# Optimization experiments

Hardware: AMD Instinct MI355X
Metric: run time of the kernel (lower is better)

Reference implementation:

```python
import jax, jax.numpy as jnp
import numpy as np
from jax import lax

TAU = 2.0          # spikingjelly LIFNode default tau
VTH = 1.0          # v_threshold
ALPHA = 2.0        # ATan surrogate alpha (grad only; fwd is heaviside)
N_WIN = (2, 4, 4)
TOPK = 4
HEADS = 8
EPS = 1e-5


@jax.custom_vjp
def spike(x):
    return (x >= 0).astype(x.dtype)

def _spike_fwd(x):
    return (x >= 0).astype(x.dtype), x

def _spike_bwd(x, g):
    sg = (ALPHA / 2.0) / (1.0 + (jnp.pi / 2.0 * ALPHA * x) ** 2)
    return (g * sg,)

spike.defvjp(_spike_fwd, _spike_bwd)


def lif(x_seq):
    # multi-step LIF, v_reset=None (soft reset), decay_input=True, detach_reset
    def step(v, x):
        v = v + (x - v) / TAU
        s = spike(v - VTH)
        v = v - lax.stop_gradient(s) * VTH
        return v, s
    v0 = jnp.zeros_like(x_seq[0])
    _, s_seq = lax.scan(step, v0, x_seq)
    return s_seq


def bn3d(x, g, b):
    # track_running_stats=False -> always batch stats; step_mode 'm' folds T into batch.
    # x: [T,B,C,Lt,Lh,Lw]; normalize per-channel over (T,B,Lt,Lh,Lw)
    ax = (0, 1, 3, 4, 5)
    m = x.mean(ax, keepdims=True)
    v = x.var(ax, keepdims=True)
    sh = (1, 1, -1, 1, 1, 1)
    return g.reshape(sh) * (x - m) * lax.rsqrt(v + EPS) + b.reshape(sh)


def bra(x, wqkv, bqkv, lepe_w, wo, bo):
    # Bi-level routing attention over 3D windows. x: [N, Lt, Lh, Lw, C]
    N, Lt, Lh, Lw, C = x.shape
    nt, nh, nw = N_WIN
    rt, rh, rw = Lt // nt, Lh // nh, Lw // nw
    R, P = nt * nh * nw, rt * rh * rw
    Dh = C // HEADS

    qkv = x @ wqkv + bqkv                       # [N,Lt,Lh,Lw,3C]
    q, k, v = jnp.split(qkv, 3, axis=-1)

    def to_reg(t):  # -> [N, R, P, C]
        t = t.reshape(N, nt, rt, nh, rh, nw, rw, C)
        return t.transpose(0, 1, 3, 5, 2, 4, 6, 7).reshape(N, R, P, C)

    def from_reg(t):  # [N,R,P,C] -> [N,Lt,Lh,Lw,C]
        t = t.reshape(N, nt, nh, nw, rt, rh, rw, C)
        return t.transpose(0, 1, 4, 2, 5, 3, 6, 7).reshape(N, Lt, Lh, Lw, C)

    qr, kr, vr = to_reg(q), to_reg(k), to_reg(v)

    # coarse routing: region means, top-k region selection
    a_r = jnp.einsum('nrc,nsc->nrs', qr.mean(2), kr.mean(2))   # [N,R,R]
    _, idx = lax.top_k(a_r, TOPK)                               # [N,R,TOPK]

    # gather selected regions' k,v: [N,R,TOPK,P,C] -> [N,R,TOPK*P,H,Dh]
    kg = jax.vmap(lambda a, i: a[i])(kr, idx)
    vg = jax.vmap(lambda a, i: a[i])(vr, idx)
    kg = kg.reshape(N, R, TOPK * P, HEADS, Dh)
    vg = vg.reshape(N, R, TOPK * P, HEADS, Dh)
    qh = qr.reshape(N, R, P, HEADS, Dh)

    logits = jnp.einsum('nrphd,nrkhd->nrhpk', qh * (Dh ** -0.5), kg)
    attn = jax.nn.softmax(logits, axis=-1)
    out = jnp.einsum('nrhpk,nrkhd->nrphd', attn, vg).reshape(N, R, P, C)
    out = from_reg(out)

    # LEPE: depthwise 3x3x3 conv on v
    v_ncdhw = v.transpose(0, 4, 1, 2, 3)
    lepe = lax.conv_general_dilated(
        v_ncdhw, lepe_w, (1, 1, 1), 'SAME', feature_group_count=C,
        dimension_numbers=('NCDHW', 'OIDHW', 'NCDHW'))
    out = out + lepe.transpose(0, 2, 3, 4, 1)

    return out @ wo + bo


def setup_inputs() -> dict:
    key = jax.random.key(0)
    ks = jax.random.split(key, 8)
    T, B, C, Lt, Lh, Lw = 2, 1, 256, 8, 32, 32
    inp = {
        'x': jax.random.normal(ks[0], (T, B, C, Lt, Lh, Lw), jnp.float32),
        'bn1_g': jnp.ones((C,), jnp.float32),
        'bn1_b': jnp.zeros((C,), jnp.float32),
        'wqkv': jax.random.normal(ks[1], (C, 3 * C), jnp.float32) * (C ** -0.5),
        'bqkv': jnp.zeros((3 * C,), jnp.float32),
        'lepe_w': jax.random.normal(ks[2], (C, 1, 3, 3, 3), jnp.float32) * 0.1,
        'wo': jax.random.normal(ks[3], (C, C), jnp.float32) * (C ** -0.5),
        'bo': jnp.zeros((C,), jnp.float32),
        'bn2_g': jnp.ones((C,), jnp.float32),
        'bn2_b': jnp.zeros((C,), jnp.float32),
        'ffn_w1': jax.random.normal(ks[4], (C, 4 * C), jnp.float32) * (C ** -0.5),
        'ffn_b1': jnp.zeros((4 * C,), jnp.float32),
        'ffn_w2': jax.random.normal(ks[5], (4 * C, C), jnp.float32) * ((4 * C) ** -0.5),
        'ffn_b2': jnp.zeros((C,), jnp.float32),
        'scale': jnp.ones((1,), jnp.float32) * 0.5,
    }
    return inp


def reference(x, bn1_g, bn1_b, wqkv, bqkv, lepe_w, wo, bo,
              bn2_g, bn2_b, ffn_w1, ffn_b1, ffn_w2, ffn_b2, scale):
    T, B, C, Lt, Lh, Lw = x.shape

    # --- attention branch ---
    s1 = lif(bn3d(x, bn1_g, bn1_b))                       # [T,B,C,Lt,Lh,Lw]
    sa = s1.transpose(0, 1, 3, 4, 5, 2).reshape(T * B, Lt, Lh, Lw, C)
    a = bra(sa, wqkv, bqkv, lepe_w, wo, bo)
    a = a.reshape(T, B, Lt, Lh, Lw, C).transpose(0, 1, 5, 2, 3, 4)
    x = x + a * scale

    # --- FFN branch (1x1x1 conv = channel GEMM) ---
    s2 = lif(bn3d(x, bn2_g, bn2_b))
    h = jax.nn.gelu(jnp.einsum('tbcdhw,cf->tbfdhw', s2, ffn_w1)
                    + ffn_b1.reshape(1, 1, -1, 1, 1, 1), approximate=False)
    f = (jnp.einsum('tbfdhw,fc->tbcdhw', h, ffn_w2)
         + ffn_b2.reshape(1, 1, -1, 1, 1, 1))
    return x + f * scale
```

## Files before the change

kernel.cpp:

```cpp
#include <hip/hip_runtime.h>
#include <math.h>

#define CC 256
#define LL 8192
#define RR 32
#define PPP 256
#define NTOP 4
#define TOKS 16384
#define TBLK (TOKS * 32)

typedef unsigned short u16;
typedef __attribute__((ext_vector_type(8))) short short8;
typedef __attribute__((ext_vector_type(8))) unsigned short u16x8;
typedef __attribute__((ext_vector_type(4))) float f32x4;
typedef __attribute__((ext_vector_type(4))) unsigned short u16x4;

#if defined(__has_builtin)
#if __has_builtin(__builtin_amdgcn_exp2f)
#define EXP2(x) __builtin_amdgcn_exp2f(x)
#endif
#endif
#ifndef EXP2
#define EXP2(x) exp2f(x)
#endif

__device__ inline u16 f2bf(float f) {
  unsigned int b = __float_as_uint(f);
  unsigned int r = (b + 0x7FFFu + ((b >> 16) & 1u)) >> 16;
  return (u16)r;
}
__device__ inline float bf2f(u16 x) { return __uint_as_float(((unsigned int)x) << 16); }

__global__ __launch_bounds__(256) void k_bnstats(const float* __restrict__ x,
                                                 float* __restrict__ mean,
                                                 float* __restrict__ istd) {
  int c = blockIdx.x, tid = threadIdx.x;
  float s = 0.f, sq = 0.f;
  for (int i = tid; i < 2 * LL / 4; i += 256) {
    int t = i >> 11, l4 = (i & 2047) * 4;
    float4 v = *(const float4*)&x[(size_t)(t * CC + c) * LL + l4];
    s += (v.x + v.y) + (v.z + v.w);
    sq += (v.x * v.x + v.y * v.y) + (v.z * v.z + v.w * v.w);
  }
  __shared__ float rs[256], rq[256];
  rs[tid] = s; rq[tid] = sq;
  __syncthreads();
  for (int off = 128; off > 0; off >>= 1) {
    if (tid < off) { rs[tid] += rs[tid + off]; rq[tid] += rq[tid + off]; }
    __syncthreads();
  }
  if (tid == 0) {
    float m = rs[0] * (1.f / (2 * LL));
    float var = rq[0] * (1.f / (2 * LL)) - m * m;
    mean[c] = m;
    istd[c] = rsqrtf(var + 1e-5f);
  }
}

__global__ __launch_bounds__(128) void k_bnfin(const float* __restrict__ psum,
                                               const float* __restrict__ psq,
                                               float* __restrict__ mean,
                                               float* __restrict__ istd) {
  int c = blockIdx.x;
  int tid = threadIdx.x;
  __shared__ float rs[128], rq[128];
  rs[tid] = psum[c * 128 + tid];
  rq[tid] = psq[c * 128 + tid];
  __syncthreads();
  for (int off = 64; off > 0; off >>= 1) {
    if (tid < off) { rs[tid] += rs[tid + off]; rq[tid] += rq[tid + off]; }
    __syncthreads();
  }
  if (tid == 0) {
    float m = rs[0] * (1.f / 16384.f);
    float var = rq[0] * (1.f / 16384.f) - m * m;
    mean[c] = m;
    istd[c] = rsqrtf(var + 1e-5f);
  }
}

__global__ __launch_bounds__(256) void k_lifT(const float* __restrict__ xin,
                                              const float* __restrict__ mean,
                                              const float* __restrict__ istd,
                                              const float* __restrict__ g,
                                              const float* __restrict__ b,
                                              u16* __restrict__ actT) {
  __shared__ float t0[32][33], t1[32][33];
  int l0 = blockIdx.x * 32, c0 = blockIdx.y * 32;
  int tx = threadIdx.x & 31, ty = threadIdx.x >> 5;
  for (int i = 0; i < 32; i += 8) {
    int c = c0 + ty + i;
    float m = mean[c], is = istd[c], gg = g[c], bb = b[c];
    float x0 = xin[(size_t)c * LL + l0 + tx];
    float x1 = xin[(size_t)(CC + c) * LL + l0 + tx];
    float y0 = gg * (x0 - m) * is + bb;
    float y1 = gg * (x1 - m) * is + bb;
    float v = y0 * 0.5f;
    float s0 = (v >= 1.f) ? 1.f : 0.f;
    v -= s0;
    v += (y1 - v) * 0.5f;
    float s1 = (v >= 1.f) ? 1.f : 0.f;
    t0[ty + i][tx] = s0;
    t1[ty + i][tx] = s1;
  }
  __syncthreads();
  size_t kb = (size_t)(c0 >> 5) * TBLK;
  for (int i = 0; i < 32; i += 8) {
    int l = l0 + ty + i;
    actT[kb + (size_t)l * 32 + tx] = f2bf(t0[tx][ty + i]);
    actT[kb + (size_t)(LL + l) * 32 + tx] = f2bf(t1[tx][ty + i]);
  }
}

__device__ inline void tr_tile(const float* __restrict__ in, u16* __restrict__ out,
                               int C, int c0, int r0) {
  __shared__ float t[32][33];
  int tx = threadIdx.x & 31, ty = threadIdx.x >> 5;
  for (int i = 0; i < 32; i += 8)
    t[ty + i][tx] = in[(size_t)(r0 + ty + i) * C + c0 + tx];
  __syncthreads();
  size_t kb = (size_t)(r0 >> 5) * C * 32;
  for (int i = 0; i < 32; i += 8)
    out[kb + (size_t)(c0 + ty + i) * 32 + tx] = f2bf(t[tx][ty + i]);
}

__global__ __launch_bounds__(256) void k_trall(const float* __restrict__ wqkv,
                                               const float* __restrict__ w1,
                                               const float* __restrict__ w2,
                                               const float* __restrict__ wo,
                                               const float* __restrict__ lep,
                                               u16* __restrict__ wqkvT, u16* __restrict__ w1T,
                                               u16* __restrict__ w2T, u16* __restrict__ woT,
                                               float* __restrict__ wTlep) {
  int b = blockIdx.x;
  if (b < 192) {
    tr_tile(wqkv, wqkvT, 768, (b % 24) * 32, (b / 24) * 32);
  } else if (b < 448) {
    int i = b - 192;
    tr_tile(w1, w1T, 1024, (i % 32) * 32, (i / 32) * 32);
  } else if (b < 704) {
    int i = b - 448;
    tr_tile(w2, w2T, 256, (i % 8) * 32, (i / 8) * 32);
  } else if (b < 768) {
    int i = b - 704;
    tr_tile(wo, woT, 256, (i % 8) * 32, (i / 8) * 32);
  } else {
    int c = threadIdx.x;
    for (int tap = 0; tap < 27; ++tap) wTlep[tap * 256 + c] = lep[c * 27 + tap];
  }
}

template<int MR, int NR, int KTOT>
__device__ inline void mfma_core_w(const u16* __restrict__ A0, int sAb,
                                   const u16* __restrict__ B0, int sBb,
                                   int wr, int wc, f32x4 acc[MR][NR]) {
  int lane = threadIdx.x & 63;
  int u = lane & 15;
  int g8 = (lane >> 4) * 8;
  const u16* Ap = A0 + (wr * MR * 16 + u) * 32 + g8;
  const u16* Bp = B0 + (wc * NR * 16 + u) * 32 + g8;
  constexpr int NKB = KTOT >> 5;
  short8 aA[MR], bA[NR], aB[MR], bB[NR];
#pragma unroll
  for (int i = 0; i < MR; ++i) aA[i] = *(const short8*)(Ap + i * 512);
#pragma unroll
  for (int j = 0; j < NR; ++j) bA[j] = *(const short8*)(Bp + j * 512);
#pragma unroll
  for (int kb = 0; kb < NKB; kb += 2) {
    if (kb + 1 < NKB) {
#pragma unroll
      for (int i = 0; i < MR; ++i) aB[i] = *(const short8*)(Ap + (size_t)(kb + 1) * sAb + i * 512);
#pragma unroll
      for (int j = 0; j < NR; ++j) bB[j] = *(const short8*)(Bp + (size_t)(kb + 1) * sBb + j * 512);
    }
#pragma unroll
    for (int i = 0; i < MR; ++i)
#pragma unroll
      for (int j = 0; j < NR; ++j)
        acc[i][j] = __builtin_amdgcn_mfma_f32_16x16x32_bf16(aA[i], bA[j], acc[i][j], 0, 0, 0);
    if (kb + 2 < NKB) {
#pragma unroll
      for (int i = 0; i < MR; ++i) aA[i] = *(const short8*)(Ap + (size_t)(kb + 2) * sAb + i * 512);
#pragma unroll
      for (int j = 0; j < NR; ++j) bA[j] = *(const short8*)(Bp + (size_t)(kb + 2) * sBb + j * 512);
    }
    if (kb + 1 < NKB) {
#pragma unroll
      for (int i = 0; i < MR; ++i)
#pragma unroll
        for (int j = 0; j < NR; ++j)
          acc[i][j] = __builtin_amdgcn_mfma_f32_16x16x32_bf16(aB[i], bB[j], acc[i][j], 0, 0, 0);
    }
  }
}

__global__ __launch_bounds__(256) void k_gqkv(const u16* __restrict__ spkT, const u16* __restrict__ wT,
                                              const float* __restrict__ bias,
                                              u16* __restrict__ qh, u16* __restrict__ kh,
                                              u16* __restrict__ vt, u16* __restrict__ vtok) {
  f32x4 acc[4][4] = {};
  int m0 = blockIdx.x * 128, n0 = blockIdx.y * 128;
  int w = threadIdx.x >> 6;
  mfma_core_w<4, 4, 256>(spkT + (size_t)m0 * 32, TBLK, wT + (size_t)n0 * 32, 768 * 32,
                         w >> 1, w & 1, acc);
  int lane = threadIdx.x & 63;
  int wr = w >> 1, wc = w & 1;
  int u = lane & 15;
  const float QSC = 0.255034865f;
#pragma unroll
  for (int i = 0; i < 4; ++i) {
    int token0 = m0 + wr * 64 + i * 16 + (lane >> 4) * 4;
    int l = token0 & (LL - 1), nb = token0 >> 13;
    int lt = l >> 10, lh = (l >> 5) & 31, lw = l & 31;
    int r = ((lt >> 2) * 4 + (lh >> 3)) * 4 + (lw >> 3);
    int p0 = ((lt & 3) * 8 + (lh & 7)) * 8 + (lw & 7);
    int nr = nb * RR + r;
#pragma unroll
    for (int j = 0; j < 4; ++j) {
      int ch = n0 + wc * 64 + j * 16 + u;
      int which = ch >> 8, c = ch & 255;
      int hh = c >> 5, dh = c & 31;
      size_t hb = ((size_t)nr * 8 + hh) * 8192;
      float bb = bias[ch];
      if (which == 0) {
#pragma unroll
        for (int reg = 0; reg < 4; ++reg)
          qh[hb + (p0 + reg) * 32 + dh] = f2bf((acc[i][j][reg] + bb) * QSC);
      } else if (which == 1) {
#pragma unroll
        for (int reg = 0; reg < 4; ++reg)
          kh[hb + (p0 + reg) * 32 + dh] = f2bf(acc[i][j][reg] + bb);
      } else {
        u16x4 pk;
#pragma unroll
        for (int reg = 0; reg < 4; ++reg) {
          u16 vb = f2bf(acc[i][j][reg] + bb);
          pk[reg] = vb;
          vtok[(size_t)(token0 + reg) * CC + c] = vb;
        }
        *(u16x4*)&vt[hb + dh * 256 + p0] = pk;
      }
    }
  }
}

__global__ __launch_bounds__(256) void k_means(const u16* __restrict__ qh, const u16* __restrict__ kh,
                                               float* __restrict__ qm, float* __restrict__ km) {
  int nrh = blockIdx.x;
  int nr = nrh >> 3, h = nrh & 7;
  int tid = threadIdx.x;
  int dh = tid & 31, pg = tid >> 5;
  size_t base = (size_t)nrh * 8192;
  float sq = 0.f, sk = 0.f;
  for (int p = pg * 32; p < pg * 32 + 32; ++p) {
    sq += bf2f(qh[base + p * 32 + dh]);
    sk += bf2f(kh[base + p * 32 + dh]);
  }
  __shared__ float rq[256], rk[256];
  rq[tid] = sq; rk[tid] = sk;
  __syncthreads();
  if (pg == 0) {
#pragma unroll
    for (int g = 1; g < 8; ++g) { sq += rq[g * 32 + dh]; sk += rk[g * 32 + dh]; }
    qm[nr * 256 + h * 32 + dh] = sq * (1.f / 256);
    km[nr * 256 + h * 32 + dh] = sk * (1.f / 256);
  }
}

__global__ __launch_bounds__(256) void k_route(const float* __restrict__ qm,
                                               const float* __restrict__ km,
                                               int* __restrict__ idx) {
  int nr = blockIdx.x;
  int n = nr >> 5;
  int tid = threadIdx.x;
  int s = tid >> 3, cg = tid & 7;
  const float* qrow = qm + nr * CC;
  const float* krow = km + (n * RR + s) * CC;
  float sum = 0.f;
  for (int c = cg * 32; c < cg * 32 + 32; ++c) sum += qrow[c] * krow[c];
  sum += __shfl_xor(sum, 1);
  sum += __shfl_xor(sum, 2);
  sum += __shfl_xor(sum, 4);
  __shared__ float ar[32];
  if (cg == 0) ar[s] = sum;
  __syncthreads();
  if (tid == 0) {
    for (int t = 0; t < NTOP; ++t) {
      float best = -1e30f; int bi = 0;
      for (int ss = 0; ss < 32; ++ss)
        if (ar[ss] > best) { best = ar[ss]; bi = ss; }
      ar[bi] = -1e30f;
      idx[nr * NTOP + t] = bi;
    }
  }
}

__global__ __launch_bounds__(256) void k_attn_mfma(const u16* __restrict__ qh,
                                                   const u16* __restrict__ kh,
                                                   const u16* __restrict__ vt,
                                                   const int* __restrict__ idx,
                                                   u16* __restrict__ oreg) {
  int h = blockIdx.x, r = blockIdx.y, n = blockIdx.z;
  int nr = n * RR + r;
  int lane = threadIdx.x & 63;
  int w = threadIdx.x >> 6;
  int u = lane & 15, g = lane >> 4;
  int swz = (u >> 1) & 3;
  __shared__ __align__(16) unsigned pl[4096];
  unsigned* plw = &pl[w * 1024];

  const u16* qb = qh + ((size_t)nr * 8 + h) * 8192;
  int q0 = w * 64;
  short8 qf[4];
#pragma unroll
  for (int f = 0; f < 4; ++f)
    qf[f] = *(const short8*)(qb + (size_t)(q0 + f * 16 + u) * 32 + g * 8);

  f32x4 accO[2][4] = {};
  float lsum[4] = {0.f, 0.f, 0.f, 0.f};
  const int* idxp = &idx[nr * NTOP];

  for (int ri = 0; ri < NTOP; ++ri) {
    int reg = idxp[ri];
    size_t rb = ((size_t)(n * RR + reg) * 8 + h) * 8192;
#pragma unroll 2
    for (int t = 0; t < 8; ++t) {
      int pb = t * 32;
      short8 kf0 = *(const short8*)(kh + rb + (size_t)(pb + u) * 32 + g * 8);
      short8 kf1 = *(const short8*)(kh + rb + (size_t)(pb + 16 + u) * 32 + g * 8);
      short8 vf0 = *(const short8*)(vt + rb + (size_t)u * 256 + pb + g * 8);
      short8 vf1 = *(const short8*)(vt + rb + (size_t)(16 + u) * 256 + pb + g * 8);

      f32x4 s0[4], s1[4];
      __builtin_amdgcn_s_setprio(1);
#pragma unroll
      for (int nf = 0; nf < 4; ++nf) {
        s0[nf] = __builtin_amdgcn_mfma_f32_16x16x32_bf16(kf0, qf[nf], (f32x4){0.f, 0.f, 0.f, 0.f}, 0, 0, 0);
        s1[nf] = __builtin_amdgcn_mfma_f32_16x16x32_bf16(kf1, qf[nf], (f32x4){0.f, 0.f, 0.f, 0.f}, 0, 0, 0);
      }
      __builtin_amdgcn_s_setprio(0);
#pragma unroll
      for (int nf = 0; nf < 4; ++nf) {
#pragma unroll
        for (int mf = 0; mf < 2; ++mf) {
          f32x4 sv = mf ? s1[nf] : s0[nf];
          float p0 = EXP2(sv[0]);
          float p1 = EXP2(sv[1]);
          float p2 = EXP2(sv[2]);
          float p3 = EXP2(sv[3]);
          lsum[nf] += (p0 + p1) + (p2 + p3);
          unsigned wA, wB;
          asm("v_cvt_pk_bf16_f32 %0, %1, %2" : "=v"(wA) : "v"(p0), "v"(p1));
          asm("v_cvt_pk_bf16_f32 %0, %1, %2" : "=v"(wB) : "v"(p2), "v"(p3));
          int bidx = (mf * 2 + (g >> 1)) ^ swz;
          *(uint2*)&plw[nf * 256 + u * 16 + bidx * 4 + (g & 1) * 2] = make_uint2(wA, wB);
        }
      }
      __builtin_amdgcn_s_setprio(1);
#pragma unroll
      for (int nf = 0; nf < 4; ++nf) {
        short8 pf = *(const short8*)&plw[nf * 256 + u * 16 + ((g ^ swz) << 2)];
        accO[0][nf] = __builtin_amdgcn_mfma_f32_16x16x32_bf16(vf0, pf, accO[0][nf], 0, 0, 0);
        accO[1][nf] = __builtin_amdgcn_mfma_f32_16x16x32_bf16(vf1, pf, accO[1][nf], 0, 0, 0);
      }
      __builtin_amdgcn_s_setprio(0);
    }
  }

#pragma unroll
  for (int nf = 0; nf < 4; ++nf) {
    lsum[nf] += __shfl_xor(lsum[nf], 16);
    lsum[nf] += __shfl_xor(lsum[nf], 32);
    float inv = 1.f / lsum[nf];
    int q = q0 + nf * 16 + u;
    int z = (((r >> 4) & 1) << 2) | ((q >> 6) & 3);
    int y = (((r >> 2) & 3) << 3) | ((q >> 3) & 7);
    int xx = ((r & 3) << 3) | (q & 7);
    int l = (z << 10) | (y << 5) | xx;
    u16* ob = &oreg[((size_t)(n * LL + l)) * CC + h * 32];
#pragma unroll
    for (int mf = 0; mf < 2; ++mf) {
      f32x4 o = mf ? accO[1][nf] : accO[0][nf];
      float a0 = o[0] * inv, a1 = o[1] * inv, a2 = o[2] * inv, a3 = o[3] * inv;
      unsigned w0, w1;
      asm("v_cvt_pk_bf16_f32 %0, %1, %2" : "=v"(w0) : "v"(a0), "v"(a1));
      asm("v_cvt_pk_bf16_f32 %0, %1, %2" : "=v"(w1) : "v"(a2), "v"(a3));
      *(uint2*)&ob[mf * 16 + g * 4] = make_uint2(w0, w1);
    }
  }
}

__global__ __launch_bounds__(256) void k_lepe(const u16* __restrict__ oreg,
                                              const u16* __restrict__ vtok,
                                              const float* __restrict__ wT,
                                              u16* __restrict__ otok) {
  int vox = threadIdx.x >> 6;
  int b = blockIdx.x * 4 + vox;
  int l = b & (LL - 1);
  int lt = l >> 10, lh = (l >> 5) & 31, lw = l & 31;
  int c4 = (threadIdx.x & 63) * 4;
  const u16* vb = vtok + (size_t)b * CC + c4;
  float lx = 0.f, ly = 0.f, lz = 0.f, lww = 0.f;
#pragma unroll
  for (int dz = -1; dz <= 1; ++dz) {
#pragma unroll
    for (int dy = -1; dy <= 1; ++dy) {
#pragma unroll
      for (int dx = -1; dx <= 1; ++dx) {
        int z = lt + dz, y = lh + dy, xx = lw + dx;
        if (z >= 0 && z < 8 && y >= 0 && y < 32 && xx >= 0 && xx < 32) {
          int tap = ((dz + 1) * 3 + (dy + 1)) * 3 + (dx + 1);
          long off = (long)(dz * 1024 + dy * 32 + dx) * CC;
          float4 w4 = *(const float4*)&wT[tap * 256 + c4];
          u16x4 v4 = *(const u16x4*)&vb[off];
          lx = fmaf(w4.x, bf2f(v4[0]), lx);
          ly = fmaf(w4.y, bf2f(v4[1]), ly);
          lz = fmaf(w4.z, bf2f(v4[2]), lz);
          lww = fmaf(w4.w, bf2f(v4[3]), lww);
        }
      }
    }
  }
  u16x4 a4 = *(const u16x4*)&oreg[(size_t)b * CC + c4];
  size_t oaddr = (size_t)(c4 >> 5) * TBLK + (size_t)b * 32 + (c4 & 31);
  *(u16x4*)&otok[oaddr] =
      (u16x4){f2bf(bf2f(a4[0]) + lx), f2bf(bf2f(a4[1]) + ly),
              f2bf(bf2f(a4[2]) + lz), f2bf(bf2f(a4[3]) + lww)};
}

__global__ __launch_bounds__(256) void k_gffn1(const u16* __restrict__ sT, const u16* __restrict__ wT,
                                               const float* __restrict__ bias, u16* __restrict__ hbuf) {
  __shared__ __align__(16) u16 ot[4 * 128 * 40];
  f32x4 acc[4][4] = {};
  int m0 = blockIdx.x * 128, n0 = blockIdx.y * 128;
  int w = threadIdx.x >> 6;
  mfma_core_w<4, 4, 256>(sT + (size_t)m0 * 32, TBLK, wT + (size_t)n0 * 32, 1024 * 32,
                         w >> 1, w & 1, acc);
  int lane = threadIdx.x & 63;
  int wr = w >> 1, wc = w & 1;
  int u = lane & 15, g = lane >> 4;
#pragma unroll
  for (int i = 0; i < 4; ++i) {
#pragma unroll
    for (int reg = 0; reg < 4; ++reg) {
      int tl = wr * 64 + i * 16 + g * 4 + reg;
#pragma unroll
      for (int j = 0; j < 4; ++j) {
        int cl = wc * 64 + j * 16 + u;
        float z = acc[i][j][reg] + bias[n0 + cl];
        float z2 = z * z;
        float ea = z * fmaf(z2, 0.1029431f, 2.3022078f);
        float t = EXP2(ea);
        float th = (t - 1.f) * __builtin_amdgcn_rcpf(t + 1.f);
        float hz = 0.5f * z;
        float gel = fmaf(hz, th, hz);
        ot[(cl >> 5) * (128 * 40) + tl * 40 + (cl & 31)] = f2bf(gel);
      }
    }
  }
  __syncthreads();
  int kb = threadIdx.x >> 6;
  int lt2 = threadIdx.x & 63;
  int tok0 = lt2 >> 2, chunk = lt2 & 3;
  u16* gdst = hbuf + ((size_t)(n0 >> 5) + kb) * TBLK + (size_t)m0 * 32;
  const u16* lsrc = &ot[kb * (128 * 40)];
#pragma unroll
  for (int it = 0; it < 8; ++it) {
    int token = it * 16 + tok0;
    *(u16x8*)(gdst + (size_t)token * 32 + chunk * 8) =
        *(const u16x8*)(lsrc + token * 40 + chunk * 8);
  }
}

__global__ __launch_bounds__(256) void k_gffn2(const u16* __restrict__ w2T, const u16* __restrict__ hb,
                                               const float* __restrict__ bias, const float* __restrict__ scale,
                                               float* __restrict__ out) {
  __shared__ f32x4 red[2][2][4][64];
  f32x4 acc[2][4] = {};
  int n0 = blockIdx.x * 128, m0 = blockIdx.y * 32;
  int w = threadIdx.x >> 6, lane = threadIdx.x & 63;
  int kh2 = w >> 1, wc = w & 1;
  mfma_core_w<2, 4, 512>(w2T + (size_t)m0 * 32 + (size_t)kh2 * 16 * (256 * 32), 256 * 32,
                         hb + (size_t)n0 * 32 + (size_t)kh2 * 16 * TBLK, TBLK,
                         0, wc, acc);
  if (w >= 2) {
#pragma unroll
    for (int i = 0; i < 2; ++i)
#pragma unroll
      for (int j = 0; j < 4; ++j)
        red[w - 2][i][j][lane] = acc[i][j];
  }
  __syncthreads();
  if (w < 2) {
#pragma unroll
    for (int i = 0; i < 2; ++i)
#pragma unroll
      for (int j = 0; j < 4; ++j)
        acc[i][j] += red[w][i][j][lane];
    float sc = scale[0];
#pragma unroll
    for (int i = 0; i < 2; ++i) {
#pragma unroll
      for (int reg = 0; reg < 4; ++reg) {
        int ch = m0 + i * 16 + (lane >> 4) * 4 + reg;
        float bb = bias[ch];
#pragma unroll
        for (int j = 0; j < 4; ++j) {
          int token = n0 + wc * 64 + j * 16 + (lane & 15);
          int t = token >> 13, l = token & (LL - 1);
          size_t oi = ((size_t)t * CC + ch) * LL + l;
          out[oi] += (acc[i][j][reg] + bb) * sc;
        }
      }
    }
  }
}

__global__ __launch_bounds__(256) void k_gwo(const u16* __restrict__ woT, const u16* __restrict__ atok,
                                             const float* __restrict__ bias, const float* __restrict__ xin,
                                             const float* __restrict__ scale, float* __restrict__ out,
                                             float* __restrict__ psum, float* __restrict__ psq) {
  __shared__ f32x4 red[2][2][4][64];
  __shared__ float lsum[2][32], lsq[2][32];
  f32x4 acc[2][4] = {};
  int n0 = blockIdx.x * 128, m0 = blockIdx.y * 32;
  int w = threadIdx.x >> 6, lane = threadIdx.x & 63;
  int kh2 = w >> 1, wc = w & 1;
  mfma_core_w<2, 4, 128>(woT + (size_t)m0 * 32 + (size_t)kh2 * 4 * (256 * 32), 256 * 32,
                         atok + (size_t)n0 * 32 + (size_t)kh2 * 4 * TBLK, TBLK,
                         0, wc, acc);
  if (w >= 2) {
#pragma unroll
    for (int i = 0; i < 2; ++i)
#pragma unroll
      for (int j = 0; j < 4; ++j)
        red[w - 2][i][j][lane] = acc[i][j];
  }
  __syncthreads();
  if (w < 2) {
    int g = lane >> 4;
    float sc = scale[0];
#pragma unroll
    for (int i = 0; i < 2; ++i)
#pragma unroll
      for (int j = 0; j < 4; ++j)
        acc[i][j] += red[w][i][j][lane];
#pragma unroll
    for (int i = 0; i < 2; ++i) {
#pragma unroll
      for (int reg = 0; reg < 4; ++reg) {
        int ch = m0 + i * 16 + g * 4 + reg;
        float bb = bias[ch];
        float s = 0.f, q = 0.f;
#pragma unroll
        for (int j = 0; j < 4; ++j) {
          int token = n0 + wc * 64 + j * 16 + (lane & 15);
          int t = token >> 13, l = token & (LL - 1);
          size_t oi = ((size_t)t * CC + ch) * LL + l;
          float v = xin[oi] + (acc[i][j][reg] + bb) * sc;
          out[oi] = v;
          s += v; q += v * v;
        }
        s += __shfl_xor(s, 1); q += __shfl_xor(q, 1);
        s += __shfl_xor(s, 2); q += __shfl_xor(q, 2);
        s += __shfl_xor(s, 4); q += __shfl_xor(q, 4);
        s += __shfl_xor(s, 8); q += __shfl_xor(q, 8);
        if ((lane & 15) == 0) {
          lsum[wc][i * 16 + g * 4 + reg] = s;
          lsq[wc][i * 16 + g * 4 + reg] = q;
        }
      }
    }
  }
  __syncthreads();
  int tid = threadIdx.x;
  if (tid < 32) {
    psum[(m0 + tid) * 128 + blockIdx.x] = lsum[0][tid] + lsum[1][tid];
    psq[(m0 + tid) * 128 + blockIdx.x] = lsq[0][tid] + lsq[1][tid];
  }
}

extern "C" void kernel_launch(void* const* d_in, const int* in_sizes, int n_in,
                              void* d_out, int out_size, void* d_ws, size_t ws_size,
                              hipStream_t stream) {
  const float* x      = (const float*)d_in[0];
  const float* bn1_g  = (const float*)d_in[1];
  const float* bn1_b  = (const float*)d_in[2];
  const float* wqkv   = (const float*)d_in[3];
  const float* bqkv   = (const float*)d_in[4];
  const float* lepe_w = (const float*)d_in[5];
  const float* wo_w   = (const float*)d_in[6];
  const float* bo     = (const float*)d_in[7];
  const float* bn2_g  = (const float*)d_in[8];
  const float* bn2_b  = (const float*)d_in[9];
  const float* ffn_w1 = (const float*)d_in[10];
  const float* ffn_b1 = (const float*)d_in[11];
  const float* ffn_w2 = (const float*)d_in[12];
  const float* ffn_b2 = (const float*)d_in[13];
  const float* scale  = (const float*)d_in[14];
  float* out = (float*)d_out;

  float* ws    = (float*)d_ws;
  u16*   actT  = (u16*)(ws + 4194304);
  u16*   qhead = (u16*)(ws + 6291456);
  u16*   khead = (u16*)(ws + 8388608);
  u16*   vthead= (u16*)(ws + 10485760);
  u16*   vtok  = (u16*)(ws + 12582912);
  u16*   oreg  = (u16*)(ws + 16777216);
  u16*   hbuf  = (u16*)(ws + 6291456);
  u16*   wqkvT = (u16*)(ws + 20971520);
  u16*   w1T   = (u16*)(ws + 21069824);
  u16*   w2T   = (u16*)(ws + 21200896);
  u16*   woT   = (u16*)(ws + 21331968);
  float* sm    = ws + 21364736;
  float* mean1 = sm;
  float* istd1 = sm + 256;
  float* mean2 = sm + 512;
  float* istd2 = sm + 768;
  float* qm    = sm + 1024;
  float* km    = sm + 1024 + 16384;
  int*   idxb  = (int*)(sm + 1024 + 32768);
  float* wTlep = sm + 1024 + 32768 + 256;
  float* psum  = sm + 1024 + 32768 + 256 + 6912;
  float* psq   = psum + 32768;

  k_trall<<<769, 256, 0, stream>>>(wqkv, ffn_w1, ffn_w2, wo_w, lepe_w,
                                   wqkvT, w1T, w2T, woT, wTlep);

  k_bnstats<<<256, 256, 0, stream>>>(x, mean1, istd1);
  k_lifT<<<dim3(256, 8), 256, 0, stream>>>(x, mean1, istd1, bn1_g, bn1_b, actT);
  k_gqkv<<<dim3(128, 6), 256, 0, stream>>>(actT, wqkvT, bqkv, qhead, khead, vthead, vtok);
  k_means<<<512, 256, 0, stream>>>(qhead, khead, qm, km);
  k_route<<<64, 256, 0, stream>>>(qm, km, idxb);
  k_attn_mfma<<<dim3(8, RR, 2), 256, 0, stream>>>(qhead, khead, vthead, idxb, oreg);
  k_lepe<<<4096, 256, 0, stream>>>(oreg, vtok, wTlep, actT);
  k_gwo<<<dim3(128, 8), 256, 0, stream>>>(woT, actT, bo, x, scale, out, psum, psq);

  k_bnfin<<<256, 128, 0, stream>>>(psum, psq, mean2, istd2);
  k_lifT<<<dim3(256, 8), 256, 0, stream>>>(out, mean2, istd2, bn2_g, bn2_b, actT);
  k_gffn1<<<dim3(128, 8), 256, 0, stream>>>(actT, w1T, ffn_b1, hbuf);
  k_gffn2<<<dim3(128, 8), 256, 0, stream>>>(w2T, hbuf, ffn_b2, scale, out);
}
```

Before: 195.4 us.

## Fuse FFN up-projection, GELU and down-projection into one kernel

Replaces the two FFN GEMM kernels with a single kernel in which each block handles 32 tokens. It loops over hidden-dimension chunks of 128, computes the up-projection with MFMA, applies GELU into shared memory, and accumulates the down-projection immediately. This removes the round trip of the 16384x1024 bf16 hidden buffer through global memory and one launch. In exchange the grid drops to 512 blocks with small 32-token tiles, operands are loaded straight from global memory with no LDS staging, and there are two block barriers per chunk, which may lower MFMA efficiency and increase weight re-reads.

Result: faster. 189.3 us (-3.1%).

```diff
diff --git a/kernel.cpp b/kernel.cpp
--- a/kernel.cpp
+++ b/kernel.cpp
@@ -428,89 +428,83 @@
               f2bf(bf2f(a4[2]) + lz), f2bf(bf2f(a4[3]) + lww)};
 }
 
-__global__ __launch_bounds__(256) void k_gffn1(const u16* __restrict__ sT, const u16* __restrict__ wT,
-                                               const float* __restrict__ bias, u16* __restrict__ hbuf) {
-  __shared__ __align__(16) u16 ot[4 * 128 * 40];
-  f32x4 acc[4][4] = {};
-  int m0 = blockIdx.x * 128, n0 = blockIdx.y * 128;
-  int w = threadIdx.x >> 6;
-  mfma_core_w<4, 4, 256>(sT + (size_t)m0 * 32, TBLK, wT + (size_t)n0 * 32, 1024 * 32,
-                         w >> 1, w & 1, acc);
-  int lane = threadIdx.x & 63;
-  int wr = w >> 1, wc = w & 1;
+__global__ __launch_bounds__(256) void k_gffn(const u16* __restrict__ sT, const u16* __restrict__ w1T,
+                                              const u16* __restrict__ w2T,
+                                              const float* __restrict__ b1, const float* __restrict__ b2,
+                                              const float* __restrict__ scale, float* __restrict__ out) {
+  __shared__ __align__(16) u16 hl[4][32][40];
+  int m0 = blockIdx.x * 32;
+  int w = threadIdx.x >> 6, lane = threadIdx.x & 63;
   int u = lane & 15, g = lane >> 4;
+  int g8 = g * 8;
+  f32x4 acc2[4][4] = {};
+
+  const u16* ApS = sT + (size_t)(m0 + u) * 32 + g8;
+  const u16* Ap2 = w2T + (size_t)(w * 64 + u) * 32 + g8;
+
+  for (int hc = 0; hc < 8; ++hc) {
+    f32x4 acc1[2][2] = {};
+    const u16* Bp1 = w1T + (size_t)(hc * 128 + w * 32 + u) * 32 + g8;
+#pragma unroll
+    for (int kb = 0; kb < 8; ++kb) {
+      short8 a0 = *(const short8*)(ApS + (size_t)kb * TBLK);
+      short8 a1 = *(const short8*)(ApS + (size_t)kb * TBLK + 512);
+      short8 b0 = *(const short8*)(Bp1 + (size_t)kb * (1024 * 32));
+      short8 bq = *(const short8*)(Bp1 + (size_t)kb * (1024 * 32) + 512);
+      acc1[0][0] = __builtin_amdgcn_mfma_f32_16x16x32_bf16(a0, b0, acc1[0][0], 0, 0, 0);
+      acc1[0][1] = __builtin_amdgcn_mfma_f32_16x16x32_bf16(a0, bq, acc1[0][1], 0, 0, 0);
+      acc1[1][0] = __builtin_amdgcn_mfma_f32_16x16x32_bf16(a1, b0, acc1[1][0], 0, 0, 0);
+      acc1[1][1] = __builtin_amdgcn_mfma_f32_16x16x32_bf16(a1, bq, acc1[1][1], 0, 0, 0);
+    }
+    __syncthreads();
+#pragma unroll
+    for (int i = 0; i < 2; ++i) {
+#pragma unroll
+      for (int reg = 0; reg < 4; ++reg) {
+        int tokl = i * 16 + g * 4 + reg;
+#pragma unroll
+        for (int j = 0; j < 2; ++j) {
+          int hh2 = j * 16 + u;
+          float z = acc1[i][j][reg] + b1[hc * 128 + w * 32 + hh2];
+          float z2 = z * z;
+          float ea = z * fmaf(z2, 0.1029431f, 2.3022078f);
+          float t = EXP2(ea);
+          float th = (t - 1.f) * __builtin_amdgcn_rcpf(t + 1.f);
+          float hz = 0.5f * z;
+          hl[w][tokl][hh2] = f2bf(fmaf(hz, th, hz));
+        }
+      }
+    }
+    __syncthreads();
+#pragma unroll
+    for (int kb2 = 0; kb2 < 4; ++kb2) {
+      const u16* a2 = Ap2 + (size_t)(hc * 4 + kb2) * (256 * 32);
+      short8 af[4], bf2[2];
+#pragma unroll
+      for (int i = 0; i < 4; ++i) af[i] = *(const short8*)(a2 + i * 512);
+#pragma unroll
+      for (int j = 0; j < 2; ++j) bf2[j] = *(const short8*)&hl[kb2][j * 16 + u][g8];
+#pragma unroll
+      for (int i = 0; i < 4; ++i)
+#pragma unroll
+        for (int j = 0; j < 2; ++j)
+          acc2[i][j] = __builtin_amdgcn_mfma_f32_16x16x32_bf16(af[i], bf2[j], acc2[i][j], 0, 0, 0);
+    }
+  }
+
+  float sc = scale[0];
 #pragma unroll
   for (int i = 0; i < 4; ++i) {
 #pragma unroll
     for (int reg = 0; reg < 4; ++reg) {
-      int tl = wr * 64 + i * 16 + g * 4 + reg;
-#pragma unroll
-      for (int j = 0; j < 4; ++j) {
-        int cl = wc * 64 + j * 16 + u;
-        float z = acc[i][j][reg] + bias[n0 + cl];
-        float z2 = z * z;
-        float ea = z * fmaf(z2, 0.1029431f, 2.3022078f);
-        float t = EXP2(ea);
-        float th = (t - 1.f) * __builtin_amdgcn_rcpf(t + 1.f);
-        float hz = 0.5f * z;
-        float gel = fmaf(hz, th, hz);
-        ot[(cl >> 5) * (128 * 40) + tl * 40 + (cl & 31)] = f2bf(gel);
-      }
-    }
-  }
-  __syncthreads();
-  int kb = threadIdx.x >> 6;
-  int lt2 = threadIdx.x & 63;
-  int tok0 = lt2 >> 2, chunk = lt2 & 3;
-  u16* gdst = hbuf + ((size_t)(n0 >> 5) + kb) * TBLK + (size_t)m0 * 32;
-  const u16* lsrc = &ot[kb * (128 * 40)];
-#pragma unroll
-  for (int it = 0; it < 8; ++it) {
-    int token = it * 16 + tok0;
-    *(u16x8*)(gdst + (size_t)token * 32 + chunk * 8) =
-        *(const u16x8*)(lsrc + token * 40 + chunk * 8);
-  }
-}
-
-__global__ __launch_bounds__(256) void k_gffn2(const u16* __restrict__ w2T, const u16* __restrict__ hb,
-                                               const float* __restrict__ bias, const float* __restrict__ scale,
-                                               float* __restrict__ out) {
-  __shared__ f32x4 red[2][2][4][64];
-  f32x4 acc[2][4] = {};
-  int n0 = blockIdx.x * 128, m0 = blockIdx.y * 32;
-  int w = threadIdx.x >> 6, lane = threadIdx.x & 63;
-  int kh2 = w >> 1, wc = w & 1;
-  mfma_core_w<2, 4, 512>(w2T + (size_t)m0 * 32 + (size_t)kh2 * 16 * (256 * 32), 256 * 32,
-                         hb + (size_t)n0 * 32 + (size_t)kh2 * 16 * TBLK, TBLK,
-                         0, wc, acc);
-  if (w >= 2) {
-#pragma unroll
-    for (int i = 0; i < 2; ++i)
-#pragma unroll
-      for (int j = 0; j < 4; ++j)
-        red[w - 2][i][j][lane] = acc[i][j];
-  }
-  __syncthreads();
-  if (w < 2) {
-#pragma unroll
-    for (int i = 0; i < 2; ++i)
-#pragma unroll
-      for (int j = 0; j < 4; ++j)
-        acc[i][j] += red[w][i][j][lane];
-    float sc = scale[0];
-#pragma unroll
-    for (int i = 0; i < 2; ++i) {
-#pragma unroll
-      for (int reg = 0; reg < 4; ++reg) {
-        int ch = m0 + i * 16 + (lane >> 4) * 4 + reg;
-        float bb = bias[ch];
-#pragma unroll
-        for (int j = 0; j < 4; ++j) {
-          int token = n0 + wc * 64 + j * 16 + (lane & 15);
-          int t = token >> 13, l = token & (LL - 1);
-          size_t oi = ((size_t)t * CC + ch) * LL + l;
-          out[oi] += (acc[i][j][reg] + bb) * sc;
-        }
+      int ch = w * 64 + i * 16 + g * 4 + reg;
+      float bb = b2[ch];
+#pragma unroll
+      for (int j = 0; j < 2; ++j) {
+        int token = m0 + j * 16 + u;
+        int t = token >> 13, l = token & (LL - 1);
+        size_t oi = ((size_t)t * CC + ch) * LL + l;
+        out[oi] += (acc2[i][j][reg] + bb) * sc;
       }
     }
   }
@@ -607,7 +601,6 @@
   u16*   vthead= (u16*)(ws + 10485760);
   u16*   vtok  = (u16*)(ws + 12582912);
   u16*   oreg  = (u16*)(ws + 16777216);
-  u16*   hbuf  = (u16*)(ws + 6291456);
   u16*   wqkvT = (u16*)(ws + 20971520);
   u16*   w1T   = (u16*)(ws + 21069824);
   u16*   w2T   = (u16*)(ws + 21200896);
@@ -638,6 +631,5 @@
 
   k_bnfin<<<256, 128, 0, stream>>>(psum, psq, mean2, istd2);
   k_lifT<<<dim3(256, 8), 256, 0, stream>>>(out, mean2, istd2, bn2_g, bn2_b, actT);
-  k_gffn1<<<dim3(128, 8), 256, 0, stream>>>(actT, w1T, ffn_b1, hbuf);
-  k_gffn2<<<dim3(128, 8), 256, 0, stream>>>(w2T, hbuf, ffn_b2, scale, out);
-}
+  k_gffn<<<512, 256, 0, stream>>>(actT, w1T, w2T, ffn_b1, ffn_b2, scale, out);
+}
```
